# Kernel tuning notes

Measured on AMD Instinct MI355X. Metric: run time of the kernel, lower is better.

The kernel has to match this reference:

```python
import jax, jax.numpy as jnp
import numpy as np

HIDDEN = 1024
NUM_HEADS = 16
HEAD_DIM = HIDDEN // NUM_HEADS
ROPE_BASE = 10000.0


def _rope_cos_sin(seq_len, dtype):
    # inv_freq over even indices of head_dim
    inv_freq = 1.0 / (ROPE_BASE ** (jnp.arange(0, HEAD_DIM, 2, dtype=jnp.float32) / HEAD_DIM))
    t = jnp.arange(seq_len, dtype=jnp.float32)
    freqs = t[:, None] * inv_freq[None, :]            # (S, head_dim/2)
    emb = jnp.concatenate([freqs, freqs], axis=-1)    # (S, head_dim)
    cos = jnp.cos(emb)[None, None, :, :].astype(dtype)
    sin = jnp.sin(emb)[None, None, :, :].astype(dtype)
    return cos, sin


def _rotate_interleaved(x):
    # stack((-x[...,1::2], x[...,::2]), -1).flatten(-2) — interleaved pair rotation
    x1 = x[..., ::2]
    x2 = x[..., 1::2]
    return jnp.stack((-x2, x1), axis=-1).reshape(x.shape)


def _apply_rope(x, cos, sin):
    return x * cos + _rotate_interleaved(x) * sin


def setup_inputs() -> dict:
    key = jax.random.key(0)
    k0, k1, k2, k3, k4 = jax.random.split(key, 5)
    B, S = 2, 2048
    scale = 1.0 / np.sqrt(HIDDEN)
    return {
        "hidden_states": jax.random.normal(k0, (B, S, HIDDEN), dtype=jnp.float32),
        "Wq": jax.random.normal(k1, (HIDDEN, HIDDEN), dtype=jnp.float32) * scale,
        "Wk": jax.random.normal(k2, (HIDDEN, HIDDEN), dtype=jnp.float32) * scale,
        "Wv": jax.random.normal(k3, (HIDDEN, HIDDEN), dtype=jnp.float32) * scale,
        "Wo": jax.random.normal(k4, (HIDDEN, HIDDEN), dtype=jnp.float32) * scale,
    }


def reference(hidden_states, Wq, Wk, Wv, Wo):
    B, S, _ = hidden_states.shape
    # torch Linear: y = x @ W.T  (W is (out, in))
    def proj(x, W):
        y = jnp.einsum('bsd,ed->bse', x, W)
        return y.reshape(B, S, NUM_HEADS, HEAD_DIM).transpose(0, 2, 1, 3)  # (B,H,S,Dh)

    q = proj(hidden_states, Wq)
    k = proj(hidden_states, Wk)
    v = proj(hidden_states, Wv)

    cos, sin = _rope_cos_sin(S, hidden_states.dtype)
    q = _apply_rope(q, cos, sin)
    k = _apply_rope(k, cos, sin)

    scores = jnp.einsum('bhqd,bhkd->bhqk', q, k) / jnp.sqrt(jnp.asarray(HEAD_DIM, hidden_states.dtype))
    attn = jax.nn.softmax(scores, axis=-1)
    out = jnp.einsum('bhqk,bhkd->bhqd', attn, v)
    out = out.transpose(0, 2, 1, 3).reshape(B, S, HIDDEN)
    return jnp.einsum('bsd,ed->bse', out, Wo)
```

## Files before the change

### kernel.cpp

```cpp
#include <hip/hip_runtime.h>

typedef __attribute__((ext_vector_type(4)))  float  f32x4;
typedef __attribute__((ext_vector_type(16))) float  f32x16;
typedef __attribute__((ext_vector_type(8)))  short  s16x8;

__device__ __forceinline__ unsigned short f2bf(float f) {
    union { float f; unsigned u; } v; v.f = f;
    unsigned u = v.u + 0x7fffu + ((v.u >> 16) & 1u);
    return (unsigned short)(u >> 16);
}

__device__ __forceinline__ unsigned cvtpk(float lo, float hi_) {
    unsigned r;
    asm("v_cvt_pk_bf16_f32 %0, %1, %2" : "=v"(r) : "v"(lo), "v"(hi_));
    return r;
}

__device__ __forceinline__ float ex2(float x) {
#if __has_builtin(__builtin_amdgcn_exp2f)
    return __builtin_amdgcn_exp2f(x);
#else
    return exp2f(x);
#endif
}

__device__ __forceinline__ void gl_lds16(const unsigned short* g, unsigned short* l) {
    __builtin_amdgcn_global_load_lds(
        (const __attribute__((address_space(1))) void*)g,
        (__attribute__((address_space(3))) void*)l, 16, 0, 0);
}

__device__ __forceinline__ f32x4 mfma16(s16x8 a, s16x8 b, f32x4 c) {
    return __builtin_amdgcn_mfma_f32_16x16x32_bf16(a, b, c, 0, 0, 0);
}
__device__ __forceinline__ f32x16 mfma32(s16x8 a, s16x8 b, f32x16 c) {
    return __builtin_amdgcn_mfma_f32_32x32x16_bf16(a, b, c, 0, 0, 0);
}

__global__ __launch_bounds__(256) void k_prep(
    const float* __restrict__ X,  const float* __restrict__ Wq,
    const float* __restrict__ Wk, const float* __restrict__ Wv,
    const float* __restrict__ Wo,
    unsigned short* __restrict__ Xb,  unsigned short* __restrict__ Wqb,
    unsigned short* __restrict__ Wkb, unsigned short* __restrict__ Wvb,
    unsigned short* __restrict__ Wob,
    float* __restrict__ ct, float* __restrict__ st)
{
    int i = blockIdx.x * 256 + threadIdx.x;
    if (i < 2097152) {
        const float* s; unsigned short* d; int o;
        if (i < 1048576) { s = X; d = Xb; o = i; }
        else {
            int j = i - 1048576;
            int wsel = j >> 18; o = j & 262143;
            s = (wsel == 0) ? Wq : (wsel == 1) ? Wk : (wsel == 2) ? Wv : Wo;
            d = (wsel == 0) ? Wqb : (wsel == 1) ? Wkb : (wsel == 2) ? Wvb : Wob;
        }
        float4 f = reinterpret_cast<const float4*>(s)[o];
        ushort4 u;
        u.x = f2bf(f.x); u.y = f2bf(f.y); u.z = f2bf(f.z); u.w = f2bf(f.w);
        reinterpret_cast<ushort4*>(d)[o] = u;
    } else {
        int j = i - 2097152;
        int e0 = j << 2;
        int sq = e0 >> 6, d0 = e0 & 63;
        float4 cv, sv;
        #pragma unroll
        for (int k = 0; k < 4; k++) {
            int d = d0 + k;
            float invf = ex2(-(float)(d & 31) * 0.4152410118609203f);
            float ang = (float)sq * invf;
            float ss, cc;
            sincosf(ang, &ss, &cc);
            ((float*)&cv)[k] = cc; ((float*)&sv)[k] = ss;
        }
        *(float4*)&ct[e0] = cv;
        *(float4*)&st[e0] = sv;
    }
}

__global__ __launch_bounds__(256) void k_gemm_qkv(
    const unsigned short* __restrict__ Xb,
    const unsigned short* __restrict__ Wqb,
    const unsigned short* __restrict__ Wkb,
    const unsigned short* __restrict__ Wvb,
    const float* __restrict__ ct, const float* __restrict__ st,
    unsigned short* __restrict__ Qo, unsigned short* __restrict__ Ko,
    unsigned short* __restrict__ Vt)
{
    __shared__ __attribute__((aligned(16))) unsigned short As[128 * 32];
    __shared__ __attribute__((aligned(16))) unsigned short Bs[128 * 32];
    const int z = blockIdx.z;
    const int tid = threadIdx.x;
    const int lane = tid & 63;
    const int w  = tid >> 6;
    const int wm = (w >> 1) * 64, wn = (w & 1) * 64;
    const int r  = lane & 15, rg = lane >> 4;

    const unsigned short *Ap, *Bp;
    int m0, n0;
    if (z < 2) { Ap = Xb;  Bp = z ? Wkb : Wqb; m0 = blockIdx.x * 128; n0 = blockIdx.y * 128; }
    else       { Ap = Wvb; Bp = Xb;            m0 = blockIdx.y * 128; n0 = blockIdx.x * 128; }

    f32x4 acc[4][4];
    const f32x4 zf = {0.f, 0.f, 0.f, 0.f};
    #pragma unroll
    for (int i = 0; i < 4; i++)
        #pragma unroll
        for (int j = 0; j < 4; j++) acc[i][j] = zf;

    const unsigned short* ga = Ap + (size_t)(m0 + (tid >> 2)) * 1024 + (tid & 3) * 8;
    const unsigned short* gb = Bp + (size_t)(n0 + (tid >> 2)) * 1024 + (tid & 3) * 8;

    for (int k0 = 0; k0 < 1024; k0 += 32) {
        gl_lds16(ga + k0,             As + tid * 8);
        gl_lds16(ga + k0 + 64 * 1024, As + 2048 + tid * 8);
        gl_lds16(gb + k0,             Bs + tid * 8);
        gl_lds16(gb + k0 + 64 * 1024, Bs + 2048 + tid * 8);
        __syncthreads();
        s16x8 af[4], bfr[4];
        #pragma unroll
        for (int mi = 0; mi < 4; mi++) af[mi]  = *(const s16x8*)&As[(wm + mi * 16 + r) * 32 + rg * 8];
        #pragma unroll
        for (int ni = 0; ni < 4; ni++) bfr[ni] = *(const s16x8*)&Bs[(wn + ni * 16 + r) * 32 + rg * 8];
        #pragma unroll
        for (int mi = 0; mi < 4; mi++)
            #pragma unroll
            for (int ni = 0; ni < 4; ni++)
                acc[mi][ni] = mfma16(af[mi], bfr[ni], acc[mi][ni]);
        __syncthreads();
    }

    if (z < 2) {
        unsigned short* Out = z ? Ko : Qo;
        const float qscale = z ? 1.0f : 0.18033688011112042f;
        #pragma unroll
        for (int mi = 0; mi < 4; mi++)
            #pragma unroll
            for (int ni = 0; ni < 4; ni++)
                #pragma unroll
                for (int rr = 0; rr < 4; rr++) {
                    float v = acc[mi][ni][rr];
                    float vp = __shfl_xor(v, 1);
                    int m = m0 + wm + mi * 16 + rg * 4 + rr;
                    int e = n0 + wn + ni * 16 + r;
                    int s = m & 2047, d = e & 63;
                    float c = ct[(s << 6) + d], sn = st[(s << 6) + d];
                    float sgn = (e & 1) ? 1.0f : -1.0f;
                    v = fmaf(v, c, sgn * vp * sn) * qscale;
                    int b = m >> 11, h = e >> 6;
                    Out[(((size_t)(b * 16 + h) * 2048 + s) << 6) + d] = f2bf(v);
                }
    } else {
        #pragma unroll
        for (int mi = 0; mi < 4; mi++)
            #pragma unroll
            for (int ni = 0; ni < 4; ni++)
                #pragma unroll
                for (int rr = 0; rr < 4; rr++) {
                    int e  = m0 + wm + mi * 16 + rg * 4 + rr;
                    int mm = n0 + wn + ni * 16 + r;
                    int b = mm >> 11, s = mm & 2047, h = e >> 6, d = e & 63;
                    Vt[((size_t)(b * 16 + h) * 64 + d) * 2048 + s] = f2bf(acc[mi][ni][rr]);
                }
    }
}

__global__ __launch_bounds__(256, 3) void k_attn(
    const unsigned short* __restrict__ Q,
    const unsigned short* __restrict__ K,
    const unsigned short* __restrict__ Vt,
    unsigned short* __restrict__ AO)
{
    __shared__ __attribute__((aligned(16))) unsigned short Ks[2][64 * 64];
    __shared__ __attribute__((aligned(16))) unsigned short Vs[2][64 * 64];
    const int bh = blockIdx.y;
    const int q0 = blockIdx.x * 128;
    const int tid = threadIdx.x, lane = tid & 63, w = tid >> 6;
    const int ln31 = lane & 31, hi = lane >> 5;
    const int swz = (ln31 & 7) << 3;
    const unsigned short* Qp = Q  + (size_t)bh * 2048 * 64;
    const unsigned short* Kp = K  + (size_t)bh * 2048 * 64;
    const unsigned short* Vp = Vt + (size_t)bh * 64 * 2048;

    s16x8 qf[4];
    #pragma unroll
    for (int ds = 0; ds < 4; ds++)
        qf[ds] = *(const s16x8*)&Qp[(size_t)(q0 + w * 32 + ln31) * 64 + ds * 16 + hi * 8];

    f32x16 o0, o1;
    #pragma unroll
    for (int r = 0; r < 16; r++) { o0[r] = 0.f; o1[r] = 0.f; }
    float mrun = -1e30f, lrun = 0.f;

    const int c1 = tid + 256;
    const int sr0 = tid >> 3, sc0 = ((tid & 7) * 8) ^ ((sr0 & 7) << 3);
    const int sr1 = c1 >> 3,  sc1 = ((c1 & 7) * 8) ^ ((sr1 & 7) << 3);
    const unsigned short* gk0 = Kp + (size_t)sr0 * 64   + sc0;
    const unsigned short* gk1 = Kp + (size_t)sr1 * 64   + sc1;
    const unsigned short* gv0 = Vp + (size_t)sr0 * 2048 + sc0;
    const unsigned short* gv1 = Vp + (size_t)sr1 * 2048 + sc1;
    const int t80 = tid * 8, t81 = c1 * 8;

    gl_lds16(gk0, &Ks[0][t80]);
    gl_lds16(gk1, &Ks[0][t81]);
    gl_lds16(gv0, &Vs[0][t80]);
    gl_lds16(gv1, &Vs[0][t81]);
    asm volatile("s_waitcnt vmcnt(0)" ::: "memory");
    __syncthreads();

    int cur = 0;
    for (int t = 0; t < 32; ++t) {
        if (t < 31) {
            size_t ok = (size_t)(t + 1) * 4096;
            size_t ov = (size_t)(t + 1) * 64;
            gl_lds16(gk0 + ok, &Ks[cur ^ 1][t80]);
            gl_lds16(gk1 + ok, &Ks[cur ^ 1][t81]);
            gl_lds16(gv0 + ov, &Vs[cur ^ 1][t80]);
            gl_lds16(gv1 + ov, &Vs[cur ^ 1][t81]);
        }
        const unsigned short* Kb = Ks[cur];
        const unsigned short* Vb = Vs[cur];

        f32x16 s0, s1;
        #pragma unroll
        for (int r = 0; r < 16; r++) { s0[r] = 0.f; s1[r] = 0.f; }
        __builtin_amdgcn_s_setprio(1);
        #pragma unroll
        for (int ds = 0; ds < 4; ds++) {
            s16x8 k0 = *(const s16x8*)&Kb[ ln31       * 64 + ((ds * 16 + hi * 8) ^ swz)];
            s16x8 k1 = *(const s16x8*)&Kb[(32 + ln31) * 64 + ((ds * 16 + hi * 8) ^ swz)];
            s0 = mfma32(k0, qf[ds], s0);
            s1 = mfma32(k1, qf[ds], s1);
        }
        __builtin_amdgcn_s_setprio(0);

        float tm = -1e30f;
        #pragma unroll
        for (int r = 0; r < 16; r++) tm = fmaxf(tm, fmaxf(s0[r], s1[r]));
        tm = fmaxf(tm, __shfl_xor(tm, 32));
        if (!__all(tm <= mrun + 8.0f)) {
            float mnew = fmaxf(mrun, tm);
            float al = ex2(mrun - mnew);
            mrun = mnew;
            lrun *= al;
            #pragma unroll
            for (int r = 0; r < 16; r++) { o0[r] *= al; o1[r] *= al; }
        }
        float rs = 0.f;
        #pragma unroll
        for (int r = 0; r < 16; r++) { float p = ex2(s0[r] - mrun); s0[r] = p; rs += p; }
        #pragma unroll
        for (int r = 0; r < 16; r++) { float p = ex2(s1[r] - mrun); s1[r] = p; rs += p; }
        rs += __shfl_xor(rs, 32);
        lrun += rs;

        s16x8 pa[4];
        #pragma unroll
        for (int ks = 0; ks < 4; ks++) {
            float x0, x1, x2, x3, x4, x5, x6, x7;
            if      (ks == 0) { x0=s0[0]; x1=s0[1]; x2=s0[2];  x3=s0[3];  x4=s0[4];  x5=s0[5];  x6=s0[6];  x7=s0[7];  }
            else if (ks == 1) { x0=s0[8]; x1=s0[9]; x2=s0[10]; x3=s0[11]; x4=s0[12]; x5=s0[13]; x6=s0[14]; x7=s0[15]; }
            else if (ks == 2) { x0=s1[0]; x1=s1[1]; x2=s1[2];  x3=s1[3];  x4=s1[4];  x5=s1[5];  x6=s1[6];  x7=s1[7];  }
            else              { x0=s1[8]; x1=s1[9]; x2=s1[10]; x3=s1[11]; x4=s1[12]; x5=s1[13]; x6=s1[14]; x7=s1[15]; }
            unsigned a  = cvtpk(x0, x1);
            unsigned a2 = cvtpk(x2, x3);
            unsigned b  = cvtpk(x4, x5);
            unsigned b2 = cvtpk(x6, x7);
            asm volatile("v_permlane32_swap_b32 %0, %1" : "+v"(a),  "+v"(b));
            asm volatile("v_permlane32_swap_b32 %0, %1" : "+v"(a2), "+v"(b2));
            union { s16x8 v; unsigned u[4]; } pu;
            pu.u[0] = a; pu.u[1] = a2; pu.u[2] = b; pu.u[3] = b2;
            pa[ks] = pu.v;
        }

        __builtin_amdgcn_s_setprio(1);
        #pragma unroll
        for (int ks = 0; ks < 4; ks++) {
            s16x8 v0 = *(const s16x8*)&Vb[ ln31       * 64 + ((ks * 16 + hi * 8) ^ swz)];
            s16x8 v1 = *(const s16x8*)&Vb[(32 + ln31) * 64 + ((ks * 16 + hi * 8) ^ swz)];
            o0 = mfma32(v0, pa[ks], o0);
            o1 = mfma32(v1, pa[ks], o1);
        }
        __builtin_amdgcn_s_setprio(0);

        __syncthreads();
        cur ^= 1;
    }

    float inv = 1.0f / lrun;
    const int b = bh >> 4, h = bh & 15;
    const int qg = q0 + w * 32 + ln31;
    size_t base = ((size_t)(b * 2048 + qg)) * 1024 + h * 64;
    #pragma unroll
    for (int dc = 0; dc < 2; dc++) {
        #pragma unroll
        for (int g = 0; g < 4; g++) {
            float y0, y1, y2, y3;
            if (dc == 0) { y0 = o0[4*g]; y1 = o0[4*g+1]; y2 = o0[4*g+2]; y3 = o0[4*g+3]; }
            else         { y0 = o1[4*g]; y1 = o1[4*g+1]; y2 = o1[4*g+2]; y3 = o1[4*g+3]; }
            unsigned lo  = cvtpk(y0 * inv, y1 * inv);
            unsigned hi2 = cvtpk(y2 * inv, y3 * inv);
            int d = dc * 32 + 8 * g + 4 * hi;
            uint2 stv; stv.x = lo; stv.y = hi2;
            *(uint2*)&AO[base + d] = stv;
        }
    }
}

__global__ __launch_bounds__(256) void k_gemm_out(
    const unsigned short* __restrict__ AOb,
    const unsigned short* __restrict__ Wob,
    float* __restrict__ Out)
{
    __shared__ __attribute__((aligned(16))) unsigned short As[128 * 32];
    __shared__ __attribute__((aligned(16))) unsigned short Bs[128 * 32];
    const int tid = threadIdx.x;
    const int lane = tid & 63;
    const int w  = tid >> 6;
    const int wm = (w >> 1) * 64, wn = (w & 1) * 64;
    const int r  = lane & 15, rg = lane >> 4;
    const int m0 = blockIdx.x * 128, n0 = blockIdx.y * 128;

    f32x4 acc[4][4];
    const f32x4 zf = {0.f, 0.f, 0.f, 0.f};
    #pragma unroll
    for (int i = 0; i < 4; i++)
        #pragma unroll
        for (int j = 0; j < 4; j++) acc[i][j] = zf;

    const unsigned short* ga = AOb + (size_t)(m0 + (tid >> 2)) * 1024 + (tid & 3) * 8;
    const unsigned short* gb = Wob + (size_t)(n0 + (tid >> 2)) * 1024 + (tid & 3) * 8;

    for (int k0 = 0; k0 < 1024; k0 += 32) {
        gl_lds16(ga + k0,             As + tid * 8);
        gl_lds16(ga + k0 + 64 * 1024, As + 2048 + tid * 8);
        gl_lds16(gb + k0,             Bs + tid * 8);
        gl_lds16(gb + k0 + 64 * 1024, Bs + 2048 + tid * 8);
        __syncthreads();
        s16x8 af[4], bfr[4];
        #pragma unroll
        for (int mi = 0; mi < 4; mi++) af[mi]  = *(const s16x8*)&As[(wm + mi * 16 + r) * 32 + rg * 8];
        #pragma unroll
        for (int ni = 0; ni < 4; ni++) bfr[ni] = *(const s16x8*)&Bs[(wn + ni * 16 + r) * 32 + rg * 8];
        #pragma unroll
        for (int mi = 0; mi < 4; mi++)
            #pragma unroll
            for (int ni = 0; ni < 4; ni++)
                acc[mi][ni] = mfma16(af[mi], bfr[ni], acc[mi][ni]);
        __syncthreads();
    }

    #pragma unroll
    for (int mi = 0; mi < 4; mi++)
        #pragma unroll
        for (int ni = 0; ni < 4; ni++)
            #pragma unroll
            for (int rr = 0; rr < 4; rr++) {
                int m = m0 + wm + mi * 16 + rg * 4 + rr;
                int e = n0 + wn + ni * 16 + r;
                Out[(size_t)m * 1024 + e] = acc[mi][ni][rr];
            }
}

extern "C" void kernel_launch(void* const* d_in, const int* in_sizes, int n_in,
                              void* d_out, int out_size, void* d_ws, size_t ws_size,
                              hipStream_t stream) {
    const float* X  = (const float*)d_in[0];
    const float* Wq = (const float*)d_in[1];
    const float* Wk = (const float*)d_in[2];
    const float* Wv = (const float*)d_in[3];
    const float* Wo = (const float*)d_in[4];
    float* Out = (float*)d_out;
    char* ws = (char*)d_ws;

    unsigned short* Xb   = (unsigned short*)(ws);
    unsigned short* Wqb  = (unsigned short*)(ws + 8388608);
    unsigned short* Wkb  = (unsigned short*)(ws + 10485760);
    unsigned short* Wvb  = (unsigned short*)(ws + 12582912);
    unsigned short* Wob  = (unsigned short*)(ws + 14680064);
    unsigned short* Qb   = (unsigned short*)(ws + 16777216);
    unsigned short* Kb   = (unsigned short*)(ws + 25165824);
    unsigned short* Vtb  = (unsigned short*)(ws + 33554432);
    unsigned short* AOb  = (unsigned short*)(ws + 41943040);
    float*          cosT = (float*)(ws + 50331648);
    float*          sinT = (float*)(ws + 50855936);

    k_prep<<<8320, 256, 0, stream>>>(X, Wq, Wk, Wv, Wo, Xb, Wqb, Wkb, Wvb, Wob, cosT, sinT);
    k_gemm_qkv<<<dim3(32, 8, 3), 256, 0, stream>>>(Xb, Wqb, Wkb, Wvb, cosT, sinT, Qb, Kb, Vtb);
    k_attn<<<dim3(16, 32), 256, 0, stream>>>(Qb, Kb, Vtb, AOb);
    k_gemm_out<<<dim3(32, 8), 256, 0, stream>>>(AOb, Wob, Out);
}
```

Baseline: 213.0 us.

## Double-buffer GEMM LDS tiles and split attention into smaller 64-query blocks

Both projection GEMMs now keep two LDS buffers per operand. The next K-slice's global-to-LDS loads are issued before the MFMAs on the current slice, so load latency overlaps compute, and the MFMA section runs at raised wave priority. The attention kernel moves from 256-thread blocks covering 128 queries to 128-thread blocks covering 64 queries, which doubles the grid so more blocks fill the CUs. Each thread now issues four K/V tile loads instead of two. The cost is twice the GEMM LDS footprint and more redundant K/V reads across the extra attention blocks. Loop-carried buffer correctness also depends on the barrier waiting for the asynchronous LDS loads.

```diff
diff --git a/kernel.cpp b/kernel.cpp
--- a/kernel.cpp
+++ b/kernel.cpp
@@ -88,14 +88,15 @@
     unsigned short* __restrict__ Qo, unsigned short* __restrict__ Ko,
     unsigned short* __restrict__ Vt)
 {
-    __shared__ __attribute__((aligned(16))) unsigned short As[128 * 32];
-    __shared__ __attribute__((aligned(16))) unsigned short Bs[128 * 32];
+    __shared__ __attribute__((aligned(16))) unsigned short As[2][128 * 32];
+    __shared__ __attribute__((aligned(16))) unsigned short Bs[2][128 * 32];
     const int z = blockIdx.z;
     const int tid = threadIdx.x;
     const int lane = tid & 63;
     const int w  = tid >> 6;
     const int wm = (w >> 1) * 64, wn = (w & 1) * 64;
     const int r  = lane & 15, rg = lane >> 4;
+    const int t8 = tid * 8;
 
     const unsigned short *Ap, *Bp;
     int m0, n0;
@@ -112,23 +113,36 @@
     const unsigned short* ga = Ap + (size_t)(m0 + (tid >> 2)) * 1024 + (tid & 3) * 8;
     const unsigned short* gb = Bp + (size_t)(n0 + (tid >> 2)) * 1024 + (tid & 3) * 8;
 
-    for (int k0 = 0; k0 < 1024; k0 += 32) {
-        gl_lds16(ga + k0,             As + tid * 8);
-        gl_lds16(ga + k0 + 64 * 1024, As + 2048 + tid * 8);
-        gl_lds16(gb + k0,             Bs + tid * 8);
-        gl_lds16(gb + k0 + 64 * 1024, Bs + 2048 + tid * 8);
-        __syncthreads();
+    gl_lds16(ga,             &As[0][t8]);
+    gl_lds16(ga + 64 * 1024, &As[0][2048 + t8]);
+    gl_lds16(gb,             &Bs[0][t8]);
+    gl_lds16(gb + 64 * 1024, &Bs[0][2048 + t8]);
+    asm volatile("s_waitcnt vmcnt(0)" ::: "memory");
+    __syncthreads();
+
+    int cur = 0;
+    for (int k = 0; k < 32; ++k) {
+        if (k < 31) {
+            int k0 = (k + 1) * 32;
+            gl_lds16(ga + k0,             &As[cur ^ 1][t8]);
+            gl_lds16(ga + k0 + 64 * 1024, &As[cur ^ 1][2048 + t8]);
+            gl_lds16(gb + k0,             &Bs[cur ^ 1][t8]);
+            gl_lds16(gb + k0 + 64 * 1024, &Bs[cur ^ 1][2048 + t8]);
+        }
         s16x8 af[4], bfr[4];
         #pragma unroll
-        for (int mi = 0; mi < 4; mi++) af[mi]  = *(const s16x8*)&As[(wm + mi * 16 + r) * 32 + rg * 8];
-        #pragma unroll
-        for (int ni = 0; ni < 4; ni++) bfr[ni] = *(const s16x8*)&Bs[(wn + ni * 16 + r) * 32 + rg * 8];
+        for (int mi = 0; mi < 4; mi++) af[mi]  = *(const s16x8*)&As[cur][(wm + mi * 16 + r) * 32 + rg * 8];
+        #pragma unroll
+        for (int ni = 0; ni < 4; ni++) bfr[ni] = *(const s16x8*)&Bs[cur][(wn + ni * 16 + r) * 32 + rg * 8];
+        __builtin_amdgcn_s_setprio(1);
         #pragma unroll
         for (int mi = 0; mi < 4; mi++)
             #pragma unroll
             for (int ni = 0; ni < 4; ni++)
                 acc[mi][ni] = mfma16(af[mi], bfr[ni], acc[mi][ni]);
+        __builtin_amdgcn_s_setprio(0);
         __syncthreads();
+        cur ^= 1;
     }
 
     if (z < 2) {
@@ -166,7 +180,7 @@
     }
 }
 
-__global__ __launch_bounds__(256, 3) void k_attn(
+__global__ __launch_bounds__(128, 3) void k_attn(
     const unsigned short* __restrict__ Q,
     const unsigned short* __restrict__ K,
     const unsigned short* __restrict__ Vt,
@@ -175,7 +189,7 @@
     __shared__ __attribute__((aligned(16))) unsigned short Ks[2][64 * 64];
     __shared__ __attribute__((aligned(16))) unsigned short Vs[2][64 * 64];
     const int bh = blockIdx.y;
-    const int q0 = blockIdx.x * 128;
+    const int q0 = blockIdx.x * 64;
     const int tid = threadIdx.x, lane = tid & 63, w = tid >> 6;
     const int ln31 = lane & 31, hi = lane >> 5;
     const int swz = (ln31 & 7) << 3;
@@ -193,19 +207,25 @@
     for (int r = 0; r < 16; r++) { o0[r] = 0.f; o1[r] = 0.f; }
     float mrun = -1e30f, lrun = 0.f;
 
-    const int c1 = tid + 256;
-    const int sr0 = tid >> 3, sc0 = ((tid & 7) * 8) ^ ((sr0 & 7) << 3);
-    const int sr1 = c1 >> 3,  sc1 = ((c1 & 7) * 8) ^ ((sr1 & 7) << 3);
-    const unsigned short* gk0 = Kp + (size_t)sr0 * 64   + sc0;
-    const unsigned short* gk1 = Kp + (size_t)sr1 * 64   + sc1;
-    const unsigned short* gv0 = Vp + (size_t)sr0 * 2048 + sc0;
-    const unsigned short* gv1 = Vp + (size_t)sr1 * 2048 + sc1;
-    const int t80 = tid * 8, t81 = c1 * 8;
-
-    gl_lds16(gk0, &Ks[0][t80]);
-    gl_lds16(gk1, &Ks[0][t81]);
-    gl_lds16(gv0, &Vs[0][t80]);
-    gl_lds16(gv1, &Vs[0][t81]);
+    int sr[4], sc[4], tt8[4];
+    #pragma unroll
+    for (int j = 0; j < 4; j++) {
+        int c = tid + j * 128;
+        sr[j] = c >> 3;
+        sc[j] = ((c & 7) * 8) ^ ((sr[j] & 7) << 3);
+        tt8[j] = c * 8;
+    }
+    const unsigned short *gk[4], *gv[4];
+    #pragma unroll
+    for (int j = 0; j < 4; j++) {
+        gk[j] = Kp + (size_t)sr[j] * 64   + sc[j];
+        gv[j] = Vp + (size_t)sr[j] * 2048 + sc[j];
+    }
+
+    #pragma unroll
+    for (int j = 0; j < 4; j++) gl_lds16(gk[j], &Ks[0][tt8[j]]);
+    #pragma unroll
+    for (int j = 0; j < 4; j++) gl_lds16(gv[j], &Vs[0][tt8[j]]);
     asm volatile("s_waitcnt vmcnt(0)" ::: "memory");
     __syncthreads();
 
@@ -214,10 +234,10 @@
         if (t < 31) {
             size_t ok = (size_t)(t + 1) * 4096;
             size_t ov = (size_t)(t + 1) * 64;
-            gl_lds16(gk0 + ok, &Ks[cur ^ 1][t80]);
-            gl_lds16(gk1 + ok, &Ks[cur ^ 1][t81]);
-            gl_lds16(gv0 + ov, &Vs[cur ^ 1][t80]);
-            gl_lds16(gv1 + ov, &Vs[cur ^ 1][t81]);
+            #pragma unroll
+            for (int j = 0; j < 4; j++) gl_lds16(gk[j] + ok, &Ks[cur ^ 1][tt8[j]]);
+            #pragma unroll
+            for (int j = 0; j < 4; j++) gl_lds16(gv[j] + ov, &Vs[cur ^ 1][tt8[j]]);
         }
         const unsigned short* Kb = Ks[cur];
         const unsigned short* Vb = Vs[cur];
@@ -313,14 +333,15 @@
     const unsigned short* __restrict__ Wob,
     float* __restrict__ Out)
 {
-    __shared__ __attribute__((aligned(16))) unsigned short As[128 * 32];
-    __shared__ __attribute__((aligned(16))) unsigned short Bs[128 * 32];
+    __shared__ __attribute__((aligned(16))) unsigned short As[2][128 * 32];
+    __shared__ __attribute__((aligned(16))) unsigned short Bs[2][128 * 32];
     const int tid = threadIdx.x;
     const int lane = tid & 63;
     const int w  = tid >> 6;
     const int wm = (w >> 1) * 64, wn = (w & 1) * 64;
     const int r  = lane & 15, rg = lane >> 4;
     const int m0 = blockIdx.x * 128, n0 = blockIdx.y * 128;
+    const int t8 = tid * 8;
 
     f32x4 acc[4][4];
     const f32x4 zf = {0.f, 0.f, 0.f, 0.f};
@@ -332,23 +353,36 @@
     const unsigned short* ga = AOb + (size_t)(m0 + (tid >> 2)) * 1024 + (tid & 3) * 8;
     const unsigned short* gb = Wob + (size_t)(n0 + (tid >> 2)) * 1024 + (tid & 3) * 8;
 
-    for (int k0 = 0; k0 < 1024; k0 += 32) {
-        gl_lds16(ga + k0,             As + tid * 8);
-        gl_lds16(ga + k0 + 64 * 1024, As + 2048 + tid * 8);
-        gl_lds16(gb + k0,             Bs + tid * 8);
-        gl_lds16(gb + k0 + 64 * 1024, Bs + 2048 + tid * 8);
-        __syncthreads();
+    gl_lds16(ga,             &As[0][t8]);
+    gl_lds16(ga + 64 * 1024, &As[0][2048 + t8]);
+    gl_lds16(gb,             &Bs[0][t8]);
+    gl_lds16(gb + 64 * 1024, &Bs[0][2048 + t8]);
+    asm volatile("s_waitcnt vmcnt(0)" ::: "memory");
+    __syncthreads();
+
+    int cur = 0;
+    for (int k = 0; k < 32; ++k) {
+        if (k < 31) {
+            int k0 = (k + 1) * 32;
+            gl_lds16(ga + k0,             &As[cur ^ 1][t8]);
+            gl_lds16(ga + k0 + 64 * 1024, &As[cur ^ 1][2048 + t8]);
+            gl_lds16(gb + k0,             &Bs[cur ^ 1][t8]);
+            gl_lds16(gb + k0 + 64 * 1024, &Bs[cur ^ 1][2048 + t8]);
+        }
         s16x8 af[4], bfr[4];
         #pragma unroll
-        for (int mi = 0; mi < 4; mi++) af[mi]  = *(const s16x8*)&As[(wm + mi * 16 + r) * 32 + rg * 8];
-        #pragma unroll
-        for (int ni = 0; ni < 4; ni++) bfr[ni] = *(const s16x8*)&Bs[(wn + ni * 16 + r) * 32 + rg * 8];
+        for (int mi = 0; mi < 4; mi++) af[mi]  = *(const s16x8*)&As[cur][(wm + mi * 16 + r) * 32 + rg * 8];
+        #pragma unroll
+        for (int ni = 0; ni < 4; ni++) bfr[ni] = *(const s16x8*)&Bs[cur][(wn + ni * 16 + r) * 32 + rg * 8];
+        __builtin_amdgcn_s_setprio(1);
         #pragma unroll
         for (int mi = 0; mi < 4; mi++)
             #pragma unroll
             for (int ni = 0; ni < 4; ni++)
                 acc[mi][ni] = mfma16(af[mi], bfr[ni], acc[mi][ni]);
+        __builtin_amdgcn_s_setprio(0);
         __syncthreads();
+        cur ^= 1;
     }
 
     #pragma unroll
@@ -388,6 +422,6 @@
 
     k_prep<<<8320, 256, 0, stream>>>(X, Wq, Wk, Wv, Wo, Xb, Wqb, Wkb, Wvb, Wob, cosT, sinT);
     k_gemm_qkv<<<dim3(32, 8, 3), 256, 0, stream>>>(Xb, Wqb, Wkb, Wvb, cosT, sinT, Qb, Kb, Vtb);
-    k_attn<<<dim3(16, 32), 256, 0, stream>>>(Qb, Kb, Vtb, AOb);
+    k_attn<<<dim3(32, 32), 128, 0, stream>>>(Qb, Kb, Vtb, AOb);
     k_gemm_out<<<dim3(32, 8), 256, 0, stream>>>(AOb, Wob, Out);
 }
```

New measurement: 234.8 us. +10.3%, slower.
